# Optimization experiments

Measured on AMD Instinct MI355X. Metric: run time of the kernel, lower is better.

## Reference

```python
import jax, jax.numpy as jnp
import numpy as np
import math

B_SZ, T_LEN, DIM = 1, 1024, 1024
D_STATE, EXPAND, NUM_SCALES, CONV_K = 16, 2, 3, 4
D_INNER = EXPAND * DIM
EPS_LOG = 1e-38
LN_EPS = 1e-5


def _causal_dwconv(x, w, b):
    # x: (B,T,D), w: (D,1,K) depthwise, b: (D,). torch Conv1d(pad=K-1)[:, :, :T] == left-pad K-1 (causal).
    y = jax.lax.conv_general_dilated(
        jnp.transpose(x, (0, 2, 1)), w, window_strides=(1,),
        padding=[(CONV_K - 1, 0)], dimension_numbers=('NCH', 'OIH', 'NCH'),
        feature_group_count=w.shape[0])
    return jnp.transpose(y, (0, 2, 1)) + b


def _ssm_core(x, cw, cb, xw, dtw, dtb, Dp):
    # x: (B,T,d_inner)
    xc = jax.nn.silu(_causal_dwconv(x, cw, cb))
    proj = xc @ xw.T                               # (B,T,2*d_state)
    B_ssm, C_ssm = proj[..., :D_STATE], proj[..., D_STATE:]
    dt = jax.nn.softplus(B_ssm @ dtw.T + dtb)      # (B,T,d_inner)
    dt = jax.nn.softplus(dt)                       # selective_scan applies softplus a second time (faithful)
    A = -jnp.arange(1, D_STATE + 1, dtype=xc.dtype)  # (d_state,) == -A_init row, same for every d_inner channel
    dA = jnp.exp(dt[..., None] * A)                # (B,T,d_inner,d_state)
    dBx = dt[..., None] * B_ssm[:, :, None, :] * xc[..., None]
    log_dA = jnp.log(jnp.clip(dA, EPS_LOG))
    log_dBx = jnp.log(jnp.clip(dBx, EPS_LOG))
    # parallel_scan_cpu: h = exp(cumsum(log_dA) + logcumsumexp(log_dBx - cumsum(log_dA)))
    a_star = jnp.cumsum(log_dA, axis=1)
    h = jnp.exp(a_star + jax.lax.cumlogsumexp(log_dBx - a_star, axis=1))
    return jnp.einsum('bts,btds->btd', C_ssm, h) + Dp * xc


def _downsample(x, stride):
    if stride == 1:
        return x
    Bb, T, D = x.shape
    Tt = (T // stride) * stride
    return x[:, :Tt].reshape(Bb, Tt // stride, stride, D).mean(2)


def _upsample(x, T_out):
    # F.interpolate(mode='linear', align_corners=False)
    T_in = x.shape[1]
    if T_in == T_out:
        return x
    scale = T_in / T_out
    pos = jnp.clip((jnp.arange(T_out, dtype=jnp.float32) + 0.5) * scale - 0.5, 0.0, T_in - 1)
    lo = jnp.floor(pos).astype(jnp.int32)
    hi = jnp.minimum(lo + 1, T_in - 1)
    w = (pos - lo.astype(pos.dtype))[None, :, None]
    return x[:, lo] * (1.0 - w) + x[:, hi] * w


def _forward(x, in_proj_w, conv_w, conv_b, xproj_w, dtproj_w, dtproj_b,
             D_param, scale_weights, gate_w1, gate_w2, out_proj_w, ln_g, ln_b):
    residual = x
    xz = x @ in_proj_w.T                           # (B,T,2*d_inner)
    x_in, gate = xz[..., :D_INNER], xz[..., D_INNER:]
    outs = []
    for s in range(NUM_SCALES):
        x_s = _downsample(x_in, 2 ** s)
        y_s = _ssm_core(x_s, conv_w[s], conv_b[s], xproj_w[s], dtproj_w[s], dtproj_b[s], D_param[s])
        outs.append(_upsample(y_s, x.shape[1]))
    w = jax.nn.softmax(scale_weights)
    fused = sum(w[s] * outs[s] for s in range(NUM_SCALES))
    ctx = sum(outs) / NUM_SCALES
    gate_ctx = jax.nn.sigmoid(jax.nn.silu(ctx @ gate_w1.T) @ gate_w2.T)
    out = (fused * gate_ctx) * jax.nn.silu(gate)
    out = out @ out_proj_w.T
    y = out + residual
    mu = y.mean(-1, keepdims=True)
    var = ((y - mu) ** 2).mean(-1, keepdims=True)
    return (y - mu) / jnp.sqrt(var + LN_EPS) * ln_g + ln_b


def setup_inputs() -> dict:
    key = jax.random.key(0)
    ks = jax.random.split(key, 12)
    g = lambda k, shp, s: (jax.random.normal(k, shp, jnp.float32) * s)
    return {
        'x': g(ks[0], (B_SZ, T_LEN, DIM), 1.0),
        'in_proj_w': g(ks[1], (2 * D_INNER, DIM), DIM ** -0.5),
        'conv_w': g(ks[2], (NUM_SCALES, D_INNER, 1, CONV_K), CONV_K ** -0.5),
        'conv_b': g(ks[3], (NUM_SCALES, D_INNER), 0.02),
        'xproj_w': g(ks[4], (NUM_SCALES, 2 * D_STATE, D_INNER), D_INNER ** -0.5),
        'dtproj_w': g(ks[5], (NUM_SCALES, D_INNER, D_STATE), D_STATE ** -0.5),
        'dtproj_b': jax.random.uniform(ks[6], (NUM_SCALES, D_INNER), jnp.float32,
                                       math.log(0.001), math.log(0.1)),
        'D_param': jnp.ones((NUM_SCALES, D_INNER), jnp.float32),
        'scale_weights': jnp.ones((NUM_SCALES,), jnp.float32) / NUM_SCALES,
        'gate_w1': g(ks[7], (D_INNER // 2, D_INNER), D_INNER ** -0.5),
        'gate_w2': g(ks[8], (D_INNER, D_INNER // 2), (D_INNER // 2) ** -0.5),
        'out_proj_w': g(ks[9], (DIM, D_INNER), D_INNER ** -0.5),
        'ln_g': jnp.ones((DIM,), jnp.float32),
        'ln_b': jnp.zeros((DIM,), jnp.float32),
    }


def reference(x, in_proj_w, conv_w, conv_b, xproj_w, dtproj_w, dtproj_b,
              D_param, scale_weights, gate_w1, gate_w2, out_proj_w, ln_g, ln_b):
    return _forward(x, in_proj_w, conv_w, conv_b, xproj_w, dtproj_w, dtproj_b,
                    D_param, scale_weights, gate_w1, gate_w2, out_proj_w, ln_g, ln_b)
```

## Files before the change

### kernel.cpp

```cpp
#include <hip/hip_runtime.h>

typedef unsigned short u16;
typedef float floatx2 __attribute__((ext_vector_type(2)));
typedef float floatx4 __attribute__((ext_vector_type(4)));
typedef short shortx8 __attribute__((ext_vector_type(8)));

#define DIN 2048

__device__ __forceinline__ u16 f2bf(float f){
  unsigned u = __float_as_uint(f);
  u = (u + 0x7fffu + ((u>>16)&1u))>>16;
  return (u16)u;
}
__device__ __forceinline__ float sigf(float x){ return 1.f/(1.f+__expf(-x)); }
__device__ __forceinline__ float siluf(float x){ return x*sigf(x); }
__device__ __forceinline__ floatx2 max2(floatx2 a, floatx2 b){
  floatx2 r; r.x = fmaxf(a.x, b.x); r.y = fmaxf(a.y, b.y); return r;
}

#define OFF_WINP  0ull
#define OFF_WG1   8388608ull
#define OFF_WG2   12582912ull
#define OFF_WOP   16777216ull
#define OFF_XB    20971520ull
#define OFF_XIN   23068672ull
#define OFF_SGATE 31457280ull
#define OFF_X1    39845888ull
#define OFF_X2    44040192ull
#define OFF_XC0   46137344ull
#define OFF_XC1   54525952ull
#define OFF_XC2   58720256ull
#define OFF_FUSED 60817408ull
#define OFF_G3O   69206016ull
#define OFF_Y0    75497472ull
#define OFF_Y1    83886080ull
#define OFF_Y2    88080384ull
#define OFF_P0    90177536ull
#define OFF_P1    90308608ull
#define OFF_P2    90374144ull
#define OFF_PS    92274688ull
#define OFF_HINIT 121634816ull
#define OFF_CTXB  OFF_XC0
#define OFF_T1B   OFF_XC1
#define OFF_T1A0  OFF_XIN
#define OFF_T1A1  OFF_X1
#define OFF_YPA0  OFF_Y1
#define OFF_YPA1  (OFF_XC0 + 4194304ull)
#define OFF_DT0   OFF_FUSED
#define OFF_DT1   OFF_G3O
#define OFF_DT2   (OFF_G3O + 4194304ull)

__device__ __forceinline__ void gld_lds16(const void* g, void* l){
  __builtin_amdgcn_global_load_lds((const __attribute__((address_space(1))) unsigned*)g,
                                   (__attribute__((address_space(3))) unsigned*)l, 16, 0, 0);
}

__global__ __launch_bounds__(256) void cvt_kernel(
    const float* __restrict__ s0, u16* __restrict__ d0,
    const float* __restrict__ s1, u16* __restrict__ d1,
    const float* __restrict__ s2, u16* __restrict__ d2,
    const float* __restrict__ s3, u16* __restrict__ d3,
    const float* __restrict__ s4, u16* __restrict__ d4)
{
  int i = (blockIdx.x*256 + threadIdx.x)*4;
  const float* s; u16* d;
  if      (i <  4194304){ s=s0; d=d0; }
  else if (i <  6291456){ s=s1; d=d1; i -=  4194304; }
  else if (i <  8388608){ s=s2; d=d2; i -=  6291456; }
  else if (i < 10485760){ s=s3; d=d3; i -=  8388608; }
  else                  { s=s4; d=d4; i -= 10485760; }
  const float4 v = *(const float4*)(s + i);
  ushort4 o; o.x = f2bf(v.x); o.y = f2bf(v.y); o.z = f2bf(v.z); o.w = f2bf(v.w);
  *(ushort4*)(d + i) = o;
}

template<int MODE, int BM>
__global__ __launch_bounds__(256) void gemm_bt(
    const u16* __restrict__ A, const u16* __restrict__ B,
    int N, int K, int Ks,
    float* __restrict__ out_f, float* __restrict__ out_f2, u16* __restrict__ out_b,
    const float* __restrict__ ex0f, const float* __restrict__ ex1f,
    float* __restrict__ ex0, float* __restrict__ ex1)
{
  constexpr int NI = BM/32;
  constexpr int IP = BM/64;
  __shared__ u16 smA[2][BM*32];
  __shared__ u16 smB[2][BM*32];
  const int tid  = threadIdx.x;
  const int m0   = blockIdx.y * BM;
  const int n0   = blockIdx.x * BM;
  const int wv   = tid >> 6;
  const int lane = tid & 63;
  const int mw   = (wv >> 1) * (BM/2);
  const int nw   = (wv & 1) * (BM/2);
  const int quad = lane >> 4;
  const int l16  = lane & 15;
  const int srow = tid >> 2;
  const int scol = (tid & 3) * 8;

  floatx4 acc[NI][NI];
#pragma unroll
  for (int i=0;i<NI;i++)
#pragma unroll
    for (int j=0;j<NI;j++) acc[i][j] = (floatx4)0.f;

  const int kStart = blockIdx.z * Ks;
  const int kEnd   = kStart + Ks;

  auto stage = [&](int buf, int k0){
#pragma unroll
    for (int p=0;p<IP;p++){
      gld_lds16(A + (size_t)(m0 + p*64 + srow)*K + k0 + scol, &smA[buf][p*2048 + wv*512]);
      gld_lds16(B + (size_t)(n0 + p*64 + srow)*K + k0 + scol, &smB[buf][p*2048 + wv*512]);
    }
  };

  stage(0, kStart);
  int cur = 0;
  for (int k0 = kStart; k0 < kEnd; k0 += 32) {
    __syncthreads();
    if (k0 + 32 < kEnd) stage(cur^1, k0+32);
    shortx8 af[NI], bfr[NI];
#pragma unroll
    for (int i=0;i<NI;i++){
      af[i]  = *(const shortx8*)&smA[cur][(mw + i*16 + l16)*32 + quad*8];
      bfr[i] = *(const shortx8*)&smB[cur][(nw + i*16 + l16)*32 + quad*8];
    }
#pragma unroll
    for (int i=0;i<NI;i++)
#pragma unroll
      for (int j=0;j<NI;j++)
        acc[i][j] = __builtin_amdgcn_mfma_f32_16x16x32_bf16(af[i], bfr[j], acc[i][j], 0, 0, 0);
    cur ^= 1;
  }

#pragma unroll
  for (int i=0;i<NI;i++){
    const int mb = m0 + mw + i*16 + quad*4;
#pragma unroll
    for (int j=0;j<NI;j++){
      const int n = n0 + nw + j*16 + l16;
      const floatx4 v4 = acc[i][j];
      if (MODE == 0){
        if (n < 2048){
#pragma unroll
          for (int r=0;r<4;r++) out_f[(size_t)(mb+r)*2048 + n] = v4[r];
          ex0[(size_t)(mb>>1)*2048 + n]       = 0.5f*(v4[0]+v4[1]);
          ex0[(size_t)((mb>>1)+1)*2048 + n]   = 0.5f*(v4[2]+v4[3]);
          ex1[(size_t)(mb>>2)*2048 + n]       = 0.25f*(v4[0]+v4[1]+v4[2]+v4[3]);
        } else {
#pragma unroll
          for (int r=0;r<4;r++) out_f2[(size_t)(mb+r)*2048 + (n-2048)] = siluf(v4[r]);
        }
      } else if (MODE == 2){
#pragma unroll
        for (int r=0;r<4;r++){
          const size_t idx = (size_t)(mb+r)*N + n;
          out_b[idx] = f2bf(sigf(v4[r]) * ex0f[idx] * ex1f[idx]);
        }
      } else {
        float* dst = blockIdx.z ? out_f2 : out_f;
#pragma unroll
        for (int r=0;r<4;r++) dst[(size_t)(mb+r)*N + n] = v4[r];
      }
    }
  }
}

__global__ __launch_bounds__(256) void g2_epi(const float* __restrict__ a,
    const float* __restrict__ b, u16* __restrict__ o){
  const int i = (blockIdx.x*256 + threadIdx.x)*4;
  const float4 va = *(const float4*)(a+i);
  const float4 vb = *(const float4*)(b+i);
  ushort4 r;
  r.x = f2bf(siluf(va.x+vb.x)); r.y = f2bf(siluf(va.y+vb.y));
  r.z = f2bf(siluf(va.z+vb.z)); r.w = f2bf(siluf(va.w+vb.w));
  *(ushort4*)(o+i) = r;
}

__global__ __launch_bounds__(256) void conv_kernel(const float* __restrict__ xin,
    const float* __restrict__ x1, const float* __restrict__ x2,
    const float* __restrict__ cw, const float* __restrict__ cb,
    float* __restrict__ xc0, float* __restrict__ xc1, float* __restrict__ xc2){
  const int idx = blockIdx.x*256 + threadIdx.x;
  const float* xs; float* xc; int s, local;
  if (idx < 1024*DIN)              { s=0; local=idx;             xs=xin; xc=xc0; }
  else if (idx < (1024+512)*DIN)   { s=1; local=idx-1024*DIN;    xs=x1;  xc=xc1; }
  else                             { s=2; local=idx-1536*DIN;    xs=x2;  xc=xc2; }
  const int t = local >> 11, d = local & 2047;
  const float* w = cw + ((size_t)(s*DIN) + d)*4;
  float acc = cb[s*DIN + d];
#pragma unroll
  for (int j=0;j<4;j++){
    const int tt = t - 3 + j;
    if (tt >= 0) acc += w[j] * xs[(size_t)tt*DIN + d];
  }
  xc[local] = siluf(acc);
}

__global__ __launch_bounds__(256) void xproj_kernel(const float* __restrict__ xc0,
    const float* __restrict__ xc1, const float* __restrict__ xc2,
    const float* __restrict__ xw,
    float* __restrict__ p0, float* __restrict__ p1, float* __restrict__ p2){
  __shared__ float srow[DIN];
  const int b = blockIdx.x;
  const float* xc; float* proj; int s, t;
  if (b < 1024)      { s=0; t=b;       xc=xc0; proj=p0; }
  else if (b < 1536) { s=1; t=b-1024;  xc=xc1; proj=p1; }
  else               { s=2; t=b-1536;  xc=xc2; proj=p2; }
  const float* xr = xc + (size_t)t*DIN;
  const int tid = threadIdx.x;
#pragma unroll
  for (int q=0;q<2;q++){
    const int k = (q*256 + tid)*4;
    *(float4*)&srow[k] = *(const float4*)&xr[k];
  }
  __syncthreads();
  const int i = tid >> 3;
  const int j = tid & 7;
  const float* w = xw + ((size_t)s*32 + i)*DIN;
  float acc = 0.f;
#pragma unroll 8
  for (int c=0;c<256;c++){
    const int k = j + 8*c;
    acc += srow[k]*w[k];
  }
  acc += __shfl_xor(acc,1); acc += __shfl_xor(acc,2); acc += __shfl_xor(acc,4);
  if (j == 0) proj[t*32 + i] = acc;
}

__global__ __launch_bounds__(128) void scan_p1(
    const float* __restrict__ xc0, const float* __restrict__ xc1, const float* __restrict__ xc2,
    const float* __restrict__ p0,  const float* __restrict__ p1,  const float* __restrict__ p2,
    const float* __restrict__ dtw, const float* __restrict__ dtb,
    float* __restrict__ dt0, float* __restrict__ dt1, float* __restrict__ dt2,
    float2* __restrict__ PS)
{
  __shared__ float sproj[16*32];
  int b = blockIdx.x;
  const float *xc, *proj; float* dto; int base, s;
  if (b < 1024)      { xc=xc0; proj=p0; dto=dt0; base=0;  s=0; }
  else if (b < 1536) { b-=1024; xc=xc1; proj=p1; dto=dt1; base=64; s=1; }
  else               { b-=1536; xc=xc2; proj=p2; dto=dt2; base=96; s=2; }
  const int chunk = b >> 4;
  const int tid   = threadIdx.x;
  const int d     = (b & 15)*128 + tid;
  const int t0    = chunk*16;
  {
    const int k = tid*4;
    *(float4*)&sproj[k] = *(const float4*)&proj[t0*32 + k];
  }
  __syncthreads();

  floatx2 w2[8];
  const floatx2* wr = (const floatx2*)(dtw + ((size_t)(s*DIN) + d)*16);
#pragma unroll
  for (int k=0;k<8;k++) w2[k] = wr[k];
  const float bias = dtb[s*DIN + d];
  const floatx2 eps2 = {1e-38f, 1e-38f};

  floatx2 H2[8];
#pragma unroll
  for (int k=0;k<8;k++) H2[k] = (floatx2)0.f;
  float S = 0.f;
  const float* xcp = xc + (size_t)t0*DIN + d;
  float* dtp = dto + (size_t)t0*DIN + d;
  for (int tt=0; tt<16; tt++){
    const float xcv = xcp[(size_t)tt*DIN];
    const floatx2* Bp2 = (const floatx2*)&sproj[tt*32];
    floatx2 zz = (floatx2)0.f;
#pragma unroll
    for (int k=0;k<8;k++) zz += Bp2[k]*w2[k];
    float z = fminf(zz.x + zz.y + bias, 60.f);
    const float E     = __expf(z);
    const float denom = 2.f + E;
    const float e     = __builtin_amdgcn_rcpf(denom);
    const float dtv   = __logf(denom);
    dtp[(size_t)tt*DIN] = dtv;
    S += dtv;
    const floatx2 c2  = {dtv*xcv, dtv*xcv};
    const floatx2 es  = {e*e, e*e};
    floatx2 ep2 = {e, e*e};
#pragma unroll
    for (int k=0;k<8;k++){
      const floatx2 dA  = max2(ep2, eps2);
      const floatx2 dBx = max2(c2*Bp2[k], eps2);
      H2[k] = dA*H2[k] + dBx;
      ep2 *= es;
    }
  }
  const float q = __expf(-S);
  const floatx2 qs = {q*q, q*q};
  floatx2 qp2 = {q, q*q};
  float2* o = PS + ((size_t)(base+chunk)*2048 + d)*16;
#pragma unroll
  for (int k=0;k<8;k++){
    float2 v0; v0.x = qp2.x; v0.y = H2[k].x; o[2*k]   = v0;
    float2 v1; v1.x = qp2.y; v1.y = H2[k].y; o[2*k+1] = v1;
    qp2 *= qs;
  }
}

__global__ __launch_bounds__(256) void scan_combine(const float2* __restrict__ PS,
                                                    float* __restrict__ Hinit){
  int id = blockIdx.x*256 + threadIdx.x;
  int base, C;
  if (id < 32768)      { base=0;  C=64; }
  else if (id < 65536) { id-=32768; base=64; C=32; }
  else                 { id-=65536; base=96; C=16; }
  const size_t off = (size_t)base*32768 + id;
  const float2* ps = PS + off;
  float* hi = Hinit + off;
  float H = 0.f;
  for (int c=0;c<C;c++){
    hi[(size_t)c*32768] = H;
    const float2 v = ps[(size_t)c*32768];
    H = v.x*H + v.y;
  }
}

__global__ __launch_bounds__(128) void scan_p2(
    const float* __restrict__ xc0, const float* __restrict__ xc1, const float* __restrict__ xc2,
    const float* __restrict__ p0,  const float* __restrict__ p1,  const float* __restrict__ p2,
    const float* __restrict__ dt0, const float* __restrict__ dt1, const float* __restrict__ dt2,
    const float* __restrict__ Hinit, const float* __restrict__ Dp_all,
    float* __restrict__ y0, float* __restrict__ y1, float* __restrict__ y2)
{
  __shared__ float sproj[16*32];
  int b = blockIdx.x;
  const float *xc, *proj, *dti; float* y; int base, s;
  if (b < 1024)      { xc=xc0; proj=p0; dti=dt0; y=y0; base=0;  s=0; }
  else if (b < 1536) { b-=1024; xc=xc1; proj=p1; dti=dt1; y=y1; base=64; s=1; }
  else               { b-=1536; xc=xc2; proj=p2; dti=dt2; y=y2; base=96; s=2; }
  const int chunk = b >> 4;
  const int tid   = threadIdx.x;
  const int d     = (b & 15)*128 + tid;
  const int t0    = chunk*16;
  {
    const int k = tid*4;
    *(float4*)&sproj[k] = *(const float4*)&proj[t0*32 + k];
  }
  __syncthreads();

  floatx2 H2[8];
  const floatx2* hi = (const floatx2*)(Hinit + ((size_t)(base+chunk)*2048 + d)*16);
#pragma unroll
  for (int k=0;k<8;k++) H2[k] = hi[k];
  const float Dv = Dp_all[s*DIN + d];
  const floatx2 eps2 = {1e-38f, 1e-38f};
  const float* xcp = xc + (size_t)t0*DIN + d;
  const float* dtp = dti + (size_t)t0*DIN + d;
  float* yp = y + (size_t)t0*DIN + d;
  for (int tt=0; tt<16; tt++){
    const float xcv = xcp[(size_t)tt*DIN];
    const float dtv = dtp[(size_t)tt*DIN];
    const floatx2* Bp2 = (const floatx2*)&sproj[tt*32];
    const float e = __expf(-dtv);
    const floatx2 c2 = {dtv*xcv, dtv*xcv};
    const floatx2 es = {e*e, e*e};
    floatx2 ep2 = {e, e*e};
    floatx2 pacc2 = (floatx2)0.f;
#pragma unroll
    for (int k=0;k<8;k++){
      const floatx2 dA  = max2(ep2, eps2);
      const floatx2 dBx = max2(c2*Bp2[k], eps2);
      H2[k] = dA*H2[k] + dBx;
      pacc2 += Bp2[8+k]*H2[k];
      ep2 *= es;
    }
    yp[(size_t)tt*DIN] = pacc2.x + pacc2.y + Dv*xcv;
  }
}

__device__ __forceinline__ float ups_read(const float* __restrict__ ys, int Tin, int t, int d){
  const float scale = (float)Tin * (1.f/1024.f);
  float pos = ((float)t + 0.5f)*scale - 0.5f;
  pos = fminf(fmaxf(pos, 0.f), (float)(Tin-1));
  const int lo = (int)floorf(pos);
  const float w = pos - (float)lo;
  const int hi = min(lo+1, Tin-1);
  return ys[(size_t)lo*DIN + d]*(1.f-w) + ys[(size_t)hi*DIN + d]*w;
}

__global__ __launch_bounds__(256) void fuse_kernel(const float* __restrict__ y0,
    const float* __restrict__ y1, const float* __restrict__ y2,
    const float* __restrict__ sw, u16* __restrict__ ctxb, float* __restrict__ fused){
  const int idx = blockIdx.x*256 + threadIdx.x;
  const int t = idx >> 11, d = idx & 2047;
  const float w0r = sw[0], w1r = sw[1], w2r = sw[2];
  const float mx = fmaxf(w0r, fmaxf(w1r, w2r));
  float e0 = __expf(w0r-mx), e1 = __expf(w1r-mx), e2 = __expf(w2r-mx);
  const float inv = 1.f/(e0+e1+e2);
  e0 *= inv; e1 *= inv; e2 *= inv;
  const float o0 = y0[idx];
  const float o1 = ups_read(y1, 512, t, d);
  const float o2 = ups_read(y2, 256, t, d);
  fused[idx] = e0*o0 + e1*o1 + e2*o2;
  ctxb[idx]  = f2bf((o0+o1+o2)*(1.f/3.f));
}

__global__ __launch_bounds__(256) void ln_kernel(const float* __restrict__ ya,
    const float* __restrict__ yb, const float* __restrict__ xr,
    const float* __restrict__ g, const float* __restrict__ b, float* __restrict__ out){
  __shared__ float red[4];
  const int t = blockIdx.x;
  const size_t ro = (size_t)t*1024;
  float v[4];
  float s = 0.f;
#pragma unroll
  for (int i=0;i<4;i++){
    const int c = threadIdx.x + i*256;
    v[i] = ya[ro+c] + yb[ro+c] + xr[ro+c];
    s += v[i];
  }
  s += __shfl_xor(s,1); s += __shfl_xor(s,2); s += __shfl_xor(s,4);
  s += __shfl_xor(s,8); s += __shfl_xor(s,16); s += __shfl_xor(s,32);
  if ((threadIdx.x & 63) == 0) red[threadIdx.x>>6] = s;
  __syncthreads();
  const float mu = (red[0]+red[1]+red[2]+red[3]) * (1.f/1024.f);
  __syncthreads();
  float q = 0.f;
#pragma unroll
  for (int i=0;i<4;i++){ const float dd = v[i]-mu; q += dd*dd; }
  q += __shfl_xor(q,1); q += __shfl_xor(q,2); q += __shfl_xor(q,4);
  q += __shfl_xor(q,8); q += __shfl_xor(q,16); q += __shfl_xor(q,32);
  if ((threadIdx.x & 63) == 0) red[threadIdx.x>>6] = q;
  __syncthreads();
  const float rstd = rsqrtf((red[0]+red[1]+red[2]+red[3]) * (1.f/1024.f) + 1e-5f);
#pragma unroll
  for (int i=0;i<4;i++){
    const int c = threadIdx.x + i*256;
    out[ro + c] = (v[i]-mu)*rstd*g[c] + b[c];
  }
}

extern "C" void kernel_launch(void* const* d_in, const int* in_sizes, int n_in,
                              void* d_out, int out_size, void* d_ws, size_t ws_size,
                              hipStream_t stream) {
  const float* x     = (const float*)d_in[0];
  const float* inpw  = (const float*)d_in[1];
  const float* convw = (const float*)d_in[2];
  const float* convb = (const float*)d_in[3];
  const float* xpw   = (const float*)d_in[4];
  const float* dtw   = (const float*)d_in[5];
  const float* dtb   = (const float*)d_in[6];
  const float* Dp    = (const float*)d_in[7];
  const float* sw    = (const float*)d_in[8];
  const float* gw1   = (const float*)d_in[9];
  const float* gw2   = (const float*)d_in[10];
  const float* opw   = (const float*)d_in[11];
  const float* lng   = (const float*)d_in[12];
  const float* lnb   = (const float*)d_in[13];
  float* out = (float*)d_out;

  char* ws = (char*)d_ws;
  u16*    wInp  = (u16*)   (ws + OFF_WINP);
  u16*    wG1   = (u16*)   (ws + OFF_WG1);
  u16*    wG2   = (u16*)   (ws + OFF_WG2);
  u16*    wOp   = (u16*)   (ws + OFF_WOP);
  u16*    xb    = (u16*)   (ws + OFF_XB);
  float*  xin   = (float*) (ws + OFF_XIN);
  float*  sgate = (float*) (ws + OFF_SGATE);
  float*  x1    = (float*) (ws + OFF_X1);
  float*  x2    = (float*) (ws + OFF_X2);
  float*  xc0   = (float*) (ws + OFF_XC0);
  float*  xc1   = (float*) (ws + OFF_XC1);
  float*  xc2   = (float*) (ws + OFF_XC2);
  float*  dt0   = (float*) (ws + OFF_DT0);
  float*  dt1   = (float*) (ws + OFF_DT1);
  float*  dt2   = (float*) (ws + OFF_DT2);
  float*  y0    = (float*) (ws + OFF_Y0);
  float*  y1    = (float*) (ws + OFF_Y1);
  float*  y2    = (float*) (ws + OFF_Y2);
  float*  p0    = (float*) (ws + OFF_P0);
  float*  p1    = (float*) (ws + OFF_P1);
  float*  p2    = (float*) (ws + OFF_P2);
  float2* PS    = (float2*)(ws + OFF_PS);
  float*  Hinit = (float*) (ws + OFF_HINIT);
  u16*    ctxb  = (u16*)   (ws + OFF_CTXB);
  u16*    t1b   = (u16*)   (ws + OFF_T1B);
  float*  fused = (float*) (ws + OFF_FUSED);
  u16*    g3o   = (u16*)   (ws + OFF_G3O);
  float*  t1a0  = (float*) (ws + OFF_T1A0);
  float*  t1a1  = (float*) (ws + OFF_T1A1);
  float*  ypa0  = (float*) (ws + OFF_YPA0);
  float*  ypa1  = (float*) (ws + OFF_YPA1);

  cvt_kernel<<<11264, 256, 0, stream>>>(inpw, wInp, gw1, wG1, gw2, wG2, opw, wOp, x, xb);
  gemm_bt<0,64><<<dim3(64, 16, 1), 256, 0, stream>>>(xb, wInp, 4096, 1024, 1024,
                                                     xin, sgate, nullptr, nullptr, nullptr, x1, x2);
  conv_kernel<<<(1792*DIN)/256, 256, 0, stream>>>(xin, x1, x2, convw, convb, xc0, xc1, xc2);
  xproj_kernel<<<1792, 256, 0, stream>>>(xc0, xc1, xc2, xpw, p0, p1, p2);
  scan_p1<<<1792, 128, 0, stream>>>(xc0, xc1, xc2, p0, p1, p2, dtw, dtb,
                                    dt0, dt1, dt2, PS);
  scan_combine<<<384, 256, 0, stream>>>(PS, Hinit);
  scan_p2<<<1792, 128, 0, stream>>>(xc0, xc1, xc2, p0, p1, p2, dt0, dt1, dt2,
                                    Hinit, Dp, y0, y1, y2);
  fuse_kernel<<<(1024*DIN)/256, 256, 0, stream>>>(y0, y1, y2, sw, ctxb, fused);
  gemm_bt<4,64><<<dim3(16, 16, 2), 256, 0, stream>>>(ctxb, wG1, 1024, 2048, 1024,
                                                     t1a0, t1a1, nullptr, nullptr, nullptr, nullptr, nullptr);
  g2_epi<<<1024, 256, 0, stream>>>(t1a0, t1a1, t1b);
  gemm_bt<2,64><<<dim3(32, 16, 1), 256, 0, stream>>>(t1b, wG2, 2048, 1024, 1024,
                                                     nullptr, nullptr, g3o, fused, sgate, nullptr, nullptr);
  gemm_bt<4,64><<<dim3(16, 16, 2), 256, 0, stream>>>(g3o, wOp, 1024, 2048, 1024,
                                                     ypa0, ypa1, nullptr, nullptr, nullptr, nullptr, nullptr);
  ln_kernel<<<1024, 256, 0, stream>>>(ypa0, ypa1, x, lng, lnb, out);
}
```

Before: 300.6 us.

## Fuse causal conv into xproj and scans, recompute dt, transpose scan state layout

Removes the standalone depthwise-conv kernel. xproj_kernel, scan_p1 and scan_p2 each recompute the causal conv plus SiLU on the fly from the pre-conv activations, using a three-value sliding history per thread. scan_p2 also recomputes dt from the projection instead of reading a dt buffer that scan_p1 used to write. The chunk-state and Hinit buffers change to a channel-contiguous layout, so their stores and loads coalesce across threads. Together this removes large intermediate global writes and reads, at the cost of repeated conv and dt arithmetic, extra halo loads, and a dependence on scan_combine accepting the new layout.

After: 281.9 us. -6.2%, faster.

```diff
diff --git a/kernel.cpp b/kernel.cpp
--- a/kernel.cpp
+++ b/kernel.cpp
@@ -29,7 +29,6 @@
 #define OFF_X2    44040192ull
 #define OFF_XC0   46137344ull
 #define OFF_XC1   54525952ull
-#define OFF_XC2   58720256ull
 #define OFF_FUSED 60817408ull
 #define OFF_G3O   69206016ull
 #define OFF_Y0    75497472ull
@@ -46,9 +45,6 @@
 #define OFF_T1A1  OFF_X1
 #define OFF_YPA0  OFF_Y1
 #define OFF_YPA1  (OFF_XC0 + 4194304ull)
-#define OFF_DT0   OFF_FUSED
-#define OFF_DT1   OFF_G3O
-#define OFF_DT2   (OFF_G3O + 4194304ull)
 
 __device__ __forceinline__ void gld_lds16(const void* g, void* l){
   __builtin_amdgcn_global_load_lds((const __attribute__((address_space(1))) unsigned*)g,
@@ -178,70 +174,69 @@
   *(ushort4*)(o+i) = r;
 }
 
-__global__ __launch_bounds__(256) void conv_kernel(const float* __restrict__ xin,
+__global__ __launch_bounds__(256) void xproj_kernel(const float* __restrict__ x0,
     const float* __restrict__ x1, const float* __restrict__ x2,
     const float* __restrict__ cw, const float* __restrict__ cb,
-    float* __restrict__ xc0, float* __restrict__ xc1, float* __restrict__ xc2){
-  const int idx = blockIdx.x*256 + threadIdx.x;
-  const float* xs; float* xc; int s, local;
-  if (idx < 1024*DIN)              { s=0; local=idx;             xs=xin; xc=xc0; }
-  else if (idx < (1024+512)*DIN)   { s=1; local=idx-1024*DIN;    xs=x1;  xc=xc1; }
-  else                             { s=2; local=idx-1536*DIN;    xs=x2;  xc=xc2; }
-  const int t = local >> 11, d = local & 2047;
-  const float* w = cw + ((size_t)(s*DIN) + d)*4;
-  float acc = cb[s*DIN + d];
-#pragma unroll
-  for (int j=0;j<4;j++){
-    const int tt = t - 3 + j;
-    if (tt >= 0) acc += w[j] * xs[(size_t)tt*DIN + d];
-  }
-  xc[local] = siluf(acc);
-}
-
-__global__ __launch_bounds__(256) void xproj_kernel(const float* __restrict__ xc0,
-    const float* __restrict__ xc1, const float* __restrict__ xc2,
     const float* __restrict__ xw,
     float* __restrict__ p0, float* __restrict__ p1, float* __restrict__ p2){
   __shared__ float srow[DIN];
   const int b = blockIdx.x;
-  const float* xc; float* proj; int s, t;
-  if (b < 1024)      { s=0; t=b;       xc=xc0; proj=p0; }
-  else if (b < 1536) { s=1; t=b-1024;  xc=xc1; proj=p1; }
-  else               { s=2; t=b-1536;  xc=xc2; proj=p2; }
-  const float* xr = xc + (size_t)t*DIN;
+  const float* xs; float* proj; int s, t;
+  if (b < 1024)      { s=0; t=b;       xs=x0; proj=p0; }
+  else if (b < 1536) { s=1; t=b-1024;  xs=x1; proj=p1; }
+  else               { s=2; t=b-1536;  xs=x2; proj=p2; }
   const int tid = threadIdx.x;
 #pragma unroll
   for (int q=0;q<2;q++){
     const int k = (q*256 + tid)*4;
-    *(float4*)&srow[k] = *(const float4*)&xr[k];
+    float4 xv[4];
+#pragma unroll
+    for (int j=0;j<4;j++){
+      const int tt = t - 3 + j;
+      if (tt >= 0) xv[j] = *(const float4*)(xs + (size_t)tt*DIN + k);
+      else { xv[j].x = 0.f; xv[j].y = 0.f; xv[j].z = 0.f; xv[j].w = 0.f; }
+    }
+    const float4 w0 = *(const float4*)(cw + ((size_t)(s*DIN) + k + 0)*4);
+    const float4 w1 = *(const float4*)(cw + ((size_t)(s*DIN) + k + 1)*4);
+    const float4 w2 = *(const float4*)(cw + ((size_t)(s*DIN) + k + 2)*4);
+    const float4 w3 = *(const float4*)(cw + ((size_t)(s*DIN) + k + 3)*4);
+    const float4 cb4 = *(const float4*)(cb + (size_t)(s*DIN) + k);
+    float4 r;
+    r.x = siluf(cb4.x + w0.x*xv[0].x + w0.y*xv[1].x + w0.z*xv[2].x + w0.w*xv[3].x);
+    r.y = siluf(cb4.y + w1.x*xv[0].y + w1.y*xv[1].y + w1.z*xv[2].y + w1.w*xv[3].y);
+    r.z = siluf(cb4.z + w2.x*xv[0].z + w2.y*xv[1].z + w2.z*xv[2].z + w2.w*xv[3].z);
+    r.w = siluf(cb4.w + w3.x*xv[0].w + w3.y*xv[1].w + w3.z*xv[2].w + w3.w*xv[3].w);
+    *(float4*)&srow[k] = r;
   }
   __syncthreads();
   const int i = tid >> 3;
   const int j = tid & 7;
-  const float* w = xw + ((size_t)s*32 + i)*DIN;
+  const float4* w4 = (const float4*)(xw + ((size_t)s*32 + i)*DIN);
+  const float4* s4 = (const float4*)srow;
   float acc = 0.f;
 #pragma unroll 8
-  for (int c=0;c<256;c++){
-    const int k = j + 8*c;
-    acc += srow[k]*w[k];
+  for (int c=0;c<64;c++){
+    const float4 sv = s4[j + 8*c];
+    const float4 wv = w4[j + 8*c];
+    acc += sv.x*wv.x + sv.y*wv.y + sv.z*wv.z + sv.w*wv.w;
   }
   acc += __shfl_xor(acc,1); acc += __shfl_xor(acc,2); acc += __shfl_xor(acc,4);
   if (j == 0) proj[t*32 + i] = acc;
 }
 
 __global__ __launch_bounds__(128) void scan_p1(
-    const float* __restrict__ xc0, const float* __restrict__ xc1, const float* __restrict__ xc2,
-    const float* __restrict__ p0,  const float* __restrict__ p1,  const float* __restrict__ p2,
+    const float* __restrict__ x0, const float* __restrict__ x1, const float* __restrict__ x2,
+    const float* __restrict__ p0, const float* __restrict__ p1, const float* __restrict__ p2,
+    const float* __restrict__ cw, const float* __restrict__ cb,
     const float* __restrict__ dtw, const float* __restrict__ dtb,
-    float* __restrict__ dt0, float* __restrict__ dt1, float* __restrict__ dt2,
     float2* __restrict__ PS)
 {
   __shared__ float sproj[16*32];
   int b = blockIdx.x;
-  const float *xc, *proj; float* dto; int base, s;
-  if (b < 1024)      { xc=xc0; proj=p0; dto=dt0; base=0;  s=0; }
-  else if (b < 1536) { b-=1024; xc=xc1; proj=p1; dto=dt1; base=64; s=1; }
-  else               { b-=1536; xc=xc2; proj=p2; dto=dt2; base=96; s=2; }
+  const float *xs, *proj; int base, s;
+  if (b < 1024)      { xs=x0; proj=p0; base=0;  s=0; }
+  else if (b < 1536) { b-=1024; xs=x1; proj=p1; base=64; s=1; }
+  else               { b-=1536; xs=x2; proj=p2; base=96; s=2; }
   const int chunk = b >> 4;
   const int tid   = threadIdx.x;
   const int d     = (b & 15)*128 + tid;
@@ -252,6 +247,8 @@
   }
   __syncthreads();
 
+  const float4 wc  = *(const float4*)(cw + ((size_t)(s*DIN) + d)*4);
+  const float  cbv = cb[s*DIN + d];
   floatx2 w2[8];
   const floatx2* wr = (const floatx2*)(dtw + ((size_t)(s*DIN) + d)*16);
 #pragma unroll
@@ -263,10 +260,17 @@
 #pragma unroll
   for (int k=0;k<8;k++) H2[k] = (floatx2)0.f;
   float S = 0.f;
-  const float* xcp = xc + (size_t)t0*DIN + d;
-  float* dtp = dto + (size_t)t0*DIN + d;
+  const float* xp = xs + d;
+  float h0=0.f, h1=0.f, h2=0.f;
+  if (chunk){
+    h0 = xp[(size_t)(t0-3)*DIN];
+    h1 = xp[(size_t)(t0-2)*DIN];
+    h2 = xp[(size_t)(t0-1)*DIN];
+  }
   for (int tt=0; tt<16; tt++){
-    const float xcv = xcp[(size_t)tt*DIN];
+    const float xv  = xp[(size_t)(t0+tt)*DIN];
+    const float xcv = siluf(cbv + wc.x*h0 + wc.y*h1 + wc.z*h2 + wc.w*xv);
+    h0=h1; h1=h2; h2=xv;
     const floatx2* Bp2 = (const floatx2*)&sproj[tt*32];
     floatx2 zz = (floatx2)0.f;
 #pragma unroll
@@ -276,7 +280,6 @@
     const float denom = 2.f + E;
     const float e     = __builtin_amdgcn_rcpf(denom);
     const float dtv   = __logf(denom);
-    dtp[(size_t)tt*DIN] = dtv;
     S += dtv;
     const floatx2 c2  = {dtv*xcv, dtv*xcv};
     const floatx2 es  = {e*e, e*e};
@@ -292,11 +295,11 @@
   const float q = __expf(-S);
   const floatx2 qs = {q*q, q*q};
   floatx2 qp2 = {q, q*q};
-  float2* o = PS + ((size_t)(base+chunk)*2048 + d)*16;
+  float2* o = PS + (size_t)(base+chunk)*32768 + d;
 #pragma unroll
   for (int k=0;k<8;k++){
-    float2 v0; v0.x = qp2.x; v0.y = H2[k].x; o[2*k]   = v0;
-    float2 v1; v1.x = qp2.y; v1.y = H2[k].y; o[2*k+1] = v1;
+    float2 v0; v0.x = qp2.x; v0.y = H2[k].x; o[(size_t)(2*k  )*2048] = v0;
+    float2 v1; v1.x = qp2.y; v1.y = H2[k].y; o[(size_t)(2*k+1)*2048] = v1;
     qp2 *= qs;
   }
 }
@@ -320,18 +323,19 @@
 }
 
 __global__ __launch_bounds__(128) void scan_p2(
-    const float* __restrict__ xc0, const float* __restrict__ xc1, const float* __restrict__ xc2,
-    const float* __restrict__ p0,  const float* __restrict__ p1,  const float* __restrict__ p2,
-    const float* __restrict__ dt0, const float* __restrict__ dt1, const float* __restrict__ dt2,
+    const float* __restrict__ x0, const float* __restrict__ x1, const float* __restrict__ x2,
+    const float* __restrict__ p0, const float* __restrict__ p1, const float* __restrict__ p2,
+    const float* __restrict__ cw, const float* __restrict__ cb,
+    const float* __restrict__ dtw, const float* __restrict__ dtb,
     const float* __restrict__ Hinit, const float* __restrict__ Dp_all,
     float* __restrict__ y0, float* __restrict__ y1, float* __restrict__ y2)
 {
   __shared__ float sproj[16*32];
   int b = blockIdx.x;
-  const float *xc, *proj, *dti; float* y; int base, s;
-  if (b < 1024)      { xc=xc0; proj=p0; dti=dt0; y=y0; base=0;  s=0; }
-  else if (b < 1536) { b-=1024; xc=xc1; proj=p1; dti=dt1; y=y1; base=64; s=1; }
-  else               { b-=1536; xc=xc2; proj=p2; dti=dt2; y=y2; base=96; s=2; }
+  const float *xs, *proj; float* y; int base, s;
+  if (b < 1024)      { xs=x0; proj=p0; y=y0; base=0;  s=0; }
+  else if (b < 1536) { b-=1024; xs=x1; proj=p1; y=y1; base=64; s=1; }
+  else               { b-=1536; xs=x2; proj=p2; y=y2; base=96; s=2; }
   const int chunk = b >> 4;
   const int tid   = threadIdx.x;
   const int d     = (b & 15)*128 + tid;
@@ -342,20 +346,44 @@
   }
   __syncthreads();
 
+  const float4 wc  = *(const float4*)(cw + ((size_t)(s*DIN) + d)*4);
+  const float  cbv = cb[s*DIN + d];
+  floatx2 w2[8];
+  const floatx2* wr = (const floatx2*)(dtw + ((size_t)(s*DIN) + d)*16);
+#pragma unroll
+  for (int k=0;k<8;k++) w2[k] = wr[k];
+  const float bias = dtb[s*DIN + d];
+
   floatx2 H2[8];
-  const floatx2* hi = (const floatx2*)(Hinit + ((size_t)(base+chunk)*2048 + d)*16);
-#pragma unroll
-  for (int k=0;k<8;k++) H2[k] = hi[k];
+  const float* hi = Hinit + (size_t)(base+chunk)*32768 + d;
+#pragma unroll
+  for (int k=0;k<8;k++){
+    H2[k].x = hi[(size_t)(2*k  )*2048];
+    H2[k].y = hi[(size_t)(2*k+1)*2048];
+  }
   const float Dv = Dp_all[s*DIN + d];
   const floatx2 eps2 = {1e-38f, 1e-38f};
-  const float* xcp = xc + (size_t)t0*DIN + d;
-  const float* dtp = dti + (size_t)t0*DIN + d;
+  const float* xp = xs + d;
   float* yp = y + (size_t)t0*DIN + d;
+  float h0=0.f, h1=0.f, h2=0.f;
+  if (chunk){
+    h0 = xp[(size_t)(t0-3)*DIN];
+    h1 = xp[(size_t)(t0-2)*DIN];
+    h2 = xp[(size_t)(t0-1)*DIN];
+  }
   for (int tt=0; tt<16; tt++){
-    const float xcv = xcp[(size_t)tt*DIN];
-    const float dtv = dtp[(size_t)tt*DIN];
+    const float xv  = xp[(size_t)(t0+tt)*DIN];
+    const float xcv = siluf(cbv + wc.x*h0 + wc.y*h1 + wc.z*h2 + wc.w*xv);
+    h0=h1; h1=h2; h2=xv;
     const floatx2* Bp2 = (const floatx2*)&sproj[tt*32];
-    const float e = __expf(-dtv);
+    floatx2 zz = (floatx2)0.f;
+#pragma unroll
+    for (int k=0;k<8;k++) zz += Bp2[k]*w2[k];
+    float z = fminf(zz.x + zz.y + bias, 60.f);
+    const float E     = __expf(z);
+    const float denom = 2.f + E;
+    const float e     = __builtin_amdgcn_rcpf(denom);
+    const float dtv   = __logf(denom);
     const floatx2 c2 = {dtv*xcv, dtv*xcv};
     const floatx2 es = {e*e, e*e};
     floatx2 ep2 = {e, e*e};
@@ -463,12 +491,6 @@
   float*  sgate = (float*) (ws + OFF_SGATE);
   float*  x1    = (float*) (ws + OFF_X1);
   float*  x2    = (float*) (ws + OFF_X2);
-  float*  xc0   = (float*) (ws + OFF_XC0);
-  float*  xc1   = (float*) (ws + OFF_XC1);
-  float*  xc2   = (float*) (ws + OFF_XC2);
-  float*  dt0   = (float*) (ws + OFF_DT0);
-  float*  dt1   = (float*) (ws + OFF_DT1);
-  float*  dt2   = (float*) (ws + OFF_DT2);
   float*  y0    = (float*) (ws + OFF_Y0);
   float*  y1    = (float*) (ws + OFF_Y1);
   float*  y2    = (float*) (ws + OFF_Y2);
@@ -489,12 +511,10 @@
   cvt_kernel<<<11264, 256, 0, stream>>>(inpw, wInp, gw1, wG1, gw2, wG2, opw, wOp, x, xb);
   gemm_bt<0,64><<<dim3(64, 16, 1), 256, 0, stream>>>(xb, wInp, 4096, 1024, 1024,
                                                      xin, sgate, nullptr, nullptr, nullptr, x1, x2);
-  conv_kernel<<<(1792*DIN)/256, 256, 0, stream>>>(xin, x1, x2, convw, convb, xc0, xc1, xc2);
-  xproj_kernel<<<1792, 256, 0, stream>>>(xc0, xc1, xc2, xpw, p0, p1, p2);
-  scan_p1<<<1792, 128, 0, stream>>>(xc0, xc1, xc2, p0, p1, p2, dtw, dtb,
-                                    dt0, dt1, dt2, PS);
+  xproj_kernel<<<1792, 256, 0, stream>>>(xin, x1, x2, convw, convb, xpw, p0, p1, p2);
+  scan_p1<<<1792, 128, 0, stream>>>(xin, x1, x2, p0, p1, p2, convw, convb, dtw, dtb, PS);
   scan_combine<<<384, 256, 0, stream>>>(PS, Hinit);
-  scan_p2<<<1792, 128, 0, stream>>>(xc0, xc1, xc2, p0, p1, p2, dt0, dt1, dt2,
+  scan_p2<<<1792, 128, 0, stream>>>(xin, x1, x2, p0, p1, p2, convw, convb, dtw, dtb,
                                     Hinit, Dp, y0, y1, y2);
   fuse_kernel<<<(1024*DIN)/256, 256, 0, stream>>>(y0, y1, y2, sw, ctxb, fused);
   gemm_bt<4,64><<<dim3(16, 16, 2), 256, 0, stream>>>(ctxb, wG1, 1024, 2048, 1024,
```
